# Performance work log

Hardware: AMD Instinct MI355X
Metric: run time of the kernel (lower is better)

## Reference

```python
import jax, jax.numpy as jnp
import numpy as np

N_QUBITS = 8
N_LAYERS = 2


def _apply_1q_shared(state, U, q):
    # state: [B, 2,2,...,2]; U: [2,2] complex, applied to qubit q (axis q+1)
    state = jnp.moveaxis(state, q + 1, -1)
    state = jnp.einsum('ij,...j->...i', U, state)
    return jnp.moveaxis(state, -1, q + 1)


def _apply_1q_batched(state, U, q):
    # U: [B,2,2], per-sample gate on qubit q
    state = jnp.moveaxis(state, q + 1, -1)
    state = jnp.einsum('bij,b...j->b...i', U, state)
    return jnp.moveaxis(state, -1, q + 1)


def _apply_cnot(state, c, t):
    ca, ta = c + 1, t + 1
    s0 = jnp.take(state, 0, axis=ca)
    s1 = jnp.take(state, 1, axis=ca)
    ta_shift = ta - 1 if ta > ca else ta  # axis index after removing control axis
    s1 = jnp.flip(s1, axis=ta_shift)
    return jnp.stack([s0, s1], axis=ca)


def _rot_matrix(phi, theta, omega):
    # PennyLane Rot = RZ(omega) @ RY(theta) @ RZ(phi)
    c = jnp.cos(theta / 2).astype(jnp.complex64)
    s = jnp.sin(theta / 2).astype(jnp.complex64)
    ep = jnp.exp(-0.5j * (phi + omega).astype(jnp.complex64))
    em = jnp.exp(-0.5j * (phi - omega).astype(jnp.complex64))
    return jnp.stack([
        jnp.stack([ep * c, -jnp.conj(em) * s]),
        jnp.stack([em * s, jnp.conj(ep) * c]),
    ])


def _quantum_layer(angles, qw):
    # angles: [B, n_qubits] float; qw: [n_layers, n_qubits, 3]
    B, n = angles.shape[0], N_QUBITS
    state = jnp.zeros((B, 2 ** n), jnp.complex64).at[:, 0].set(1.0)
    state = state.reshape((B,) + (2,) * n)
    # AngleEmbedding (rotation='X'): RX(angle_q) on wire q, per-sample angle
    c = jnp.cos(angles / 2).astype(jnp.complex64)  # [B, n]
    s = (-1j * jnp.sin(angles / 2)).astype(jnp.complex64)
    for q in range(n):
        U = jnp.stack([
            jnp.stack([c[:, q], s[:, q]], -1),
            jnp.stack([s[:, q], c[:, q]], -1),
        ], -2)  # [B,2,2]
        state = _apply_1q_batched(state, U, q)
    # StronglyEntanglingLayers
    for l in range(N_LAYERS):
        for q in range(n):
            U = _rot_matrix(qw[l, q, 0], qw[l, q, 1], qw[l, q, 2])
            state = _apply_1q_shared(state, U, q)
        r = (l % (n - 1)) + 1
        for q in range(n):
            state = _apply_cnot(state, q, (q + r) % n)
    # <Z_i> expectations: wire 0 is MSB of the flattened index
    probs = jnp.abs(state.reshape(B, 2 ** n)) ** 2  # [B, 2^n]
    idx = jnp.arange(2 ** n)
    bits = (idx[None, :] >> (n - 1 - jnp.arange(n)[:, None])) & 1  # [n, 2^n]
    signs = (1.0 - 2.0 * bits).astype(probs.dtype)
    return probs @ signs.T  # [B, n]


def setup_inputs() -> dict:
    key = jax.random.key(0)
    ks = jax.random.split(key, 8)
    B, D_IN, D_OUT, H = 65536, 17, 32, 64
    x = jax.random.normal(ks[0], (B, D_IN), jnp.float32)
    Wp = jax.random.normal(ks[1], (N_QUBITS, D_IN), jnp.float32) / np.sqrt(D_IN)
    bp = jnp.zeros((N_QUBITS,), jnp.float32)
    qw = jax.random.uniform(ks[2], (N_LAYERS, N_QUBITS, 3), jnp.float32) * (2 * np.pi)
    W1 = jax.random.normal(ks[3], (H, N_QUBITS), jnp.float32) / np.sqrt(N_QUBITS)
    b1 = jnp.zeros((H,), jnp.float32)
    W2 = jax.random.normal(ks[4], (D_OUT, H), jnp.float32) / np.sqrt(H)
    b2 = jnp.zeros((D_OUT,), jnp.float32)
    return {"x": x, "Wp": Wp, "bp": bp, "qw": qw, "W1": W1, "b1": b1, "W2": W2, "b2": b2}


def reference(x, Wp, bp, qw, W1, b1, W2, b2):
    angles = x @ Wp.T + bp            # input_projection: [B, n_qubits]
    z = _quantum_layer(angles, qw)    # [B, n_qubits]
    h = jax.nn.relu(z @ W1.T + b1)    # [B, 64]
    return jnp.tanh(h @ W2.T + b2)    # [B, 32]
```

## Files before the change

kernel.cpp:

```cpp
#include <hip/hip_runtime.h>
#include <hip/hip_bf16.h>
#include <math.h>


#define DEVINL __device__ __forceinline__

struct Pau { unsigned x, z; int ph; };
constexpr int pcnt8(unsigned v){ int c=0; for(int i=0;i<8;++i) c+=(v>>i)&1; return c; }
constexpr Pau pmul(Pau a, Pau b){
  return Pau{a.x^b.x, a.z^b.z, (a.ph + b.ph + 2*pcnt8(a.z & b.x)) & 3};
}
constexpr Pau conjP(int j, int a){
  Pau X{ j<7 ? ((1u<<j)|(1u<<(j+1))) : 0x83u, 0u, 0 };
  Pau Z{ 0u, j>0 ? ((2u<<j)-1u) : 0xFEu, 0 };
  if (a==0) return X;
  if (a==2) return Z;
  Pau y = pmul(X, Z);
  return Pau{y.x, y.z, (y.ph+1)&3};
}
constexpr unsigned SQM[8] = {0x54,0xA8,0x05,0x0A,0x15,0x2A,0x55,0xAA};
constexpr int TPREF[9]   = {0,27,54,63,72,99,126,207,288};

struct TTab { unsigned char mx[288], my[288], mz[288]; signed char sg[288]; };
constexpr TTab gen_tt(){
  TTab T{};
  int t=0;
  for (int q=0;q<8;++q){
    int sup[8]={}; int m=0;
    for (int j=0;j<8;++j) if ((SQM[q]>>j)&1) sup[m++]=j;
    int nt=1; for (int i=0;i<m;++i) nt*=3;
    for (int a=0;a<nt;++a){
      Pau P{0u,0u,0}; int rem=a;
      for (int i=0;i<m;++i){ P = pmul(P, conjP(sup[i], rem%3)); rem/=3; }
      unsigned y = P.x & P.z;
      int tau = (P.ph + 3*pcnt8(y)) & 3;
      T.mx[t]=(unsigned char)(P.x & ~P.z);
      T.my[t]=(unsigned char)y;
      T.mz[t]=(unsigned char)(P.z & ~P.x);
      T.sg[t]=(signed char)(tau==0 ? 1 : -1);
      ++t;
    }
  }
  return T;
}
constexpr TTab TT = gen_tt();

struct cpx { float r, i; };
DEVINL cpx cmul(cpx a, cpx b){ return {a.r*b.r - a.i*b.i, a.r*b.i + a.i*b.r}; }
DEVINL cpx cconj(cpx a){ return {a.r, -a.i}; }
DEVINL cpx cadd(cpx a, cpx b){ return {a.r+b.r, a.i+b.i}; }

DEVINL void buildR(const float* qw3, cpx R[2][2]){
  float phi=qw3[0], th=qw3[1], om=qw3[2], s,c,sp,cp,sm,cm;
  sincosf(0.5f*th,&s,&c);
  sincosf(0.5f*(phi+om),&sp,&cp);
  sincosf(0.5f*(phi-om),&sm,&cm);
  R[0][0]={cp*c,-sp*c}; R[0][1]={-cm*s,-sm*s};
  R[1][0]={cm*s,-sm*s}; R[1][1]={cp*c, sp*c};
}
DEVINL void conjH(const cpx R[2][2], const cpx S[2][2], cpx H[2][2]){
  cpx M[2][2];
  for (int i=0;i<2;++i) for (int j=0;j<2;++j)
    M[i][j] = cadd(cmul(S[i][0],R[0][j]), cmul(S[i][1],R[1][j]));
  for (int i=0;i<2;++i) for (int j=0;j<2;++j)
    H[i][j] = cadd(cmul(cconj(R[0][i]),M[0][j]), cmul(cconj(R[1][i]),M[1][j]));
}

__global__ void prep_kernel(const float* __restrict__ qw, float* __restrict__ ws){
  __shared__ float n_sh[8][3];
  const int tid = threadIdx.x;
  if (tid < 8){
    const int q = tid;
    cpx R1[2][2], R2[2][2], H[2][2];
    buildR(qw + q*3,      R1);
    buildR(qw + 24 + q*3, R2);
    const cpx SX[2][2] = {{{0,0},{1,0}},{{1,0},{0,0}}};
    const cpx SY[2][2] = {{{0,0},{0,-1}},{{0,1},{0,0}}};
    const cpx SZ[2][2] = {{{1,0},{0,0}},{{0,0},{-1,0}}};
    conjH(R1,SX,H); ws[q*6+0] = -H[0][1].i; ws[q*6+3] = H[0][0].r;
    conjH(R1,SY,H); ws[q*6+1] = -H[0][1].i; ws[q*6+4] = H[0][0].r;
    conjH(R1,SZ,H); ws[q*6+2] = -H[0][1].i; ws[q*6+5] = H[0][0].r;
    conjH(R2,SZ,H);
    n_sh[q][0] = H[0][1].r;
    n_sh[q][1] = -H[0][1].i;
    n_sh[q][2] = H[0][0].r;
  }
  __syncthreads();
  if (tid < 288){
    int q = 0;
    while (tid >= TPREF[q+1]) ++q;
    int rem = tid - TPREF[q];
    float coef = (float)TT.sg[tid];
    unsigned m = SQM[q];
    while (m){
      int j = __ffs(m) - 1; m &= m - 1;
      coef *= n_sh[j][rem % 3];
      rem /= 3;
    }
    ws[48 + tid] = coef;
  }
}

DEVINL float tanh_fast(float v){
  float e = __expf(2.f*v);
  return 1.f - 2.f/(e + 1.f);
}

__global__ __launch_bounds__(256)
void qnet_pauli(const float* __restrict__ x, const float* __restrict__ Wp,
                const float* __restrict__ bp, const float* __restrict__ ws,
                const float* __restrict__ W1, const float* __restrict__ b1,
                const float* __restrict__ W2, const float* __restrict__ b2,
                float* __restrict__ out, int B){
  __shared__ __align__(16) float smem[3136 + 256*17];
  float* sws = smem;
  float* sWp = smem + 336;
  float* sbp = smem + 472;
  float* sW1 = smem + 480;
  float* sb1 = smem + 992;
  float* sW2 = smem + 1056;
  float* sb2 = smem + 3104;
  float* shx = smem + 3136;

  const int tid = threadIdx.x;
  const int b   = blockIdx.x*256 + tid;

  for (int i = tid; i < 336;  i += 256) sws[i] = ws[i];
  for (int i = tid; i < 136;  i += 256) sWp[i] = Wp[i];
  if (tid < 8)  sbp[tid] = bp[tid];
  for (int i = tid; i < 512;  i += 256) sW1[i] = W1[i];
  if (tid < 64) sb1[tid] = b1[tid];
  for (int i = tid; i < 2048; i += 256) sW2[i] = W2[i];
  if (tid < 32) sb2[tid] = b2[tid];

  const int base = blockIdx.x*256*17;
  const int lim  = B*17 - base;
#pragma unroll
  for (int i = 0; i < 17; ++i){
    int o = i*256 + tid;
    if (o < lim) shx[o] = x[base + o];
  }
  __syncthreads();
  if (b >= B) return;

  float rx[8], ry[8], rz[8];
  {
    float xv[17];
#pragma unroll
    for (int k=0;k<17;++k) xv[k] = shx[tid*17 + k];
#pragma unroll
    for (int q=0;q<8;++q){
      float ang = sbp[q];
#pragma unroll
      for (int k=0;k<17;++k) ang = fmaf(xv[k], sWp[q*17+k], ang);
      float sa, ca;
      __sincosf(ang, &sa, &ca);
      rx[q] = ca*sws[q*6+3] - sa*sws[q*6+0];
      ry[q] = ca*sws[q*6+4] - sa*sws[q*6+1];
      rz[q] = ca*sws[q*6+5] - sa*sws[q*6+2];
    }
  }

  const float* cf = sws + 48;
  float zz[8];
#pragma unroll
  for (int q=0;q<8;++q){
    float acc = 0.f;
#pragma unroll
    for (int t=TPREF[q]; t<TPREF[q+1]; ++t){
      float p = cf[t];
#pragma unroll
      for (int j=0;j<8;++j){
        if (TT.mx[t] & (1u<<j)) p *= rx[j];
        if (TT.my[t] & (1u<<j)) p *= ry[j];
        if (TT.mz[t] & (1u<<j)) p *= rz[j];
      }
      acc += p;
    }
    zz[q] = acc;
  }

  float acc[32];
#pragma unroll
  for (int j=0;j<32;++j) acc[j] = sb2[j];

#pragma unroll
  for (int lc=0; lc<4; ++lc){
    float h16[16];
#pragma unroll
    for (int i=0;i<16;++i){
      const int l = lc*16 + i;
      const float4* w1p = (const float4*)(sW1 + l*8);
      float4 wA = w1p[0], wB = w1p[1];
      float hl = sb1[l];
      hl = fmaf(zz[0], wA.x, hl); hl = fmaf(zz[1], wA.y, hl);
      hl = fmaf(zz[2], wA.z, hl); hl = fmaf(zz[3], wA.w, hl);
      hl = fmaf(zz[4], wB.x, hl); hl = fmaf(zz[5], wB.y, hl);
      hl = fmaf(zz[6], wB.z, hl); hl = fmaf(zz[7], wB.w, hl);
      h16[i] = fmaxf(hl, 0.f);
    }
#pragma unroll
    for (int j=0;j<32;++j){
      const float4* w2p = (const float4*)(sW2 + j*64 + lc*16);
      float4 wa = w2p[0], wb = w2p[1], wc = w2p[2], wd = w2p[3];
      float a = acc[j];
      a = fmaf(h16[ 0], wa.x, a); a = fmaf(h16[ 1], wa.y, a);
      a = fmaf(h16[ 2], wa.z, a); a = fmaf(h16[ 3], wa.w, a);
      a = fmaf(h16[ 4], wb.x, a); a = fmaf(h16[ 5], wb.y, a);
      a = fmaf(h16[ 6], wb.z, a); a = fmaf(h16[ 7], wb.w, a);
      a = fmaf(h16[ 8], wc.x, a); a = fmaf(h16[ 9], wc.y, a);
      a = fmaf(h16[10], wc.z, a); a = fmaf(h16[11], wc.w, a);
      a = fmaf(h16[12], wd.x, a); a = fmaf(h16[13], wd.y, a);
      a = fmaf(h16[14], wd.z, a); a = fmaf(h16[15], wd.w, a);
      acc[j] = a;
    }
  }

  float4* op4 = (float4*)(out + (size_t)b*32);
#pragma unroll
  for (int jj=0;jj<8;++jj){
    float4 v;
    v.x = tanh_fast(acc[jj*4+0]);
    v.y = tanh_fast(acc[jj*4+1]);
    v.z = tanh_fast(acc[jj*4+2]);
    v.w = tanh_fast(acc[jj*4+3]);
    op4[jj] = v;
  }
}

extern "C" void kernel_launch(void* const* d_in, const int* in_sizes, int n_in,
                              void* d_out, int out_size, void* d_ws, size_t ws_size,
                              hipStream_t stream) {
  const float* x  = (const float*)d_in[0];
  const float* Wp = (const float*)d_in[1];
  const float* bp = (const float*)d_in[2];
  const float* qw = (const float*)d_in[3];
  const float* W1 = (const float*)d_in[4];
  const float* b1 = (const float*)d_in[5];
  const float* W2 = (const float*)d_in[6];
  const float* b2 = (const float*)d_in[7];
  float* out = (float*)d_out;
  const int B = in_sizes[0] / 17;

  prep_kernel<<<1, 288, 0, stream>>>(qw, (float*)d_ws);
  qnet_pauli<<<(B + 255)/256, 256, 0, stream>>>(x, Wp, bp, (const float*)d_ws,
                                                W1, b1, W2, b2, out, B);
}
```

Measured before the change: 101.0 us.

## Split each sample's work across four waves with shared-memory handoff

Each block now handles 64 samples with 256 threads. The four waves each take a quarter of the angle projections, Pauli-term products, hidden units and output columns, and pass partial results through LDS between phases. Output is staged in padded LDS so global stores are coalesced. The goal is to cut per-thread register pressure, which should raise occupancy and improve store coalescing. The cost is four extra block barriers, reloading the weight tables into LDS four times as often, and more shared-memory traffic.

```diff
diff --git a/kernel.cpp b/kernel.cpp
--- a/kernel.cpp
+++ b/kernel.cpp
@@ -45,6 +45,26 @@
 }
 constexpr TTab TT = gen_tt();
 
+constexpr int qof(int t){
+  return (t<27)?0:(t<54)?1:(t<63)?2:(t<72)?3:(t<99)?4:(t<126)?5:(t<207)?6:7;
+}
+
+template<int T0, int T1>
+DEVINL void terms_range(const float* __restrict__ cf, const float rx[8],
+                        const float ry[8], const float rz[8], float zp[8]){
+#pragma unroll
+  for (int t=T0; t<T1; ++t){
+    float p = cf[t];
+#pragma unroll
+    for (int j=0;j<8;++j){
+      if (TT.mx[t] & (1u<<j)) p *= rx[j];
+      if (TT.my[t] & (1u<<j)) p *= ry[j];
+      if (TT.mz[t] & (1u<<j)) p *= rz[j];
+    }
+    zp[qof(t)] += p;
+  }
+}
+
 struct cpx { float r, i; };
 DEVINL cpx cmul(cpx a, cpx b){ return {a.r*b.r - a.i*b.i, a.r*b.i + a.i*b.r}; }
 DEVINL cpx cconj(cpx a){ return {a.r, -a.i}; }
@@ -112,120 +132,129 @@
                 const float* __restrict__ W1, const float* __restrict__ b1,
                 const float* __restrict__ W2, const float* __restrict__ b2,
                 float* __restrict__ out, int B){
-  __shared__ __align__(16) float smem[3136 + 256*17];
-  float* sws = smem;
+  __shared__ __align__(16) float smem[9536];
+  float* sA  = smem;
   float* sWp = smem + 336;
   float* sbp = smem + 472;
   float* sW1 = smem + 480;
   float* sb1 = smem + 992;
   float* sW2 = smem + 1056;
   float* sb2 = smem + 3104;
-  float* shx = smem + 3136;
+  float* X   = smem + 3136;
+  float* pzz = X;
+  float* sbl = X + 2304;
+  float* sx  = X + 3840;
+  float* sh  = X + 2304;
+  float* sout= X;
 
   const int tid = threadIdx.x;
-  const int b   = blockIdx.x*256 + tid;
-
-  for (int i = tid; i < 336;  i += 256) sws[i] = ws[i];
+  const int l   = tid & 63;
+  const int w   = tid >> 6;
+
+  for (int i = tid; i < 336;  i += 256) sA[i]  = ws[i];
   for (int i = tid; i < 136;  i += 256) sWp[i] = Wp[i];
   if (tid < 8)  sbp[tid] = bp[tid];
   for (int i = tid; i < 512;  i += 256) sW1[i] = W1[i];
   if (tid < 64) sb1[tid] = b1[tid];
   for (int i = tid; i < 2048; i += 256) sW2[i] = W2[i];
   if (tid < 32) sb2[tid] = b2[tid];
-
-  const int base = blockIdx.x*256*17;
-  const int lim  = B*17 - base;
-#pragma unroll
-  for (int i = 0; i < 17; ++i){
-    int o = i*256 + tid;
-    if (o < lim) shx[o] = x[base + o];
-  }
-  __syncthreads();
-  if (b >= B) return;
-
-  float rx[8], ry[8], rz[8];
+  const int xbase = blockIdx.x * (64*17);
+  const int xlim  = B*17 - xbase;
+  for (int i = tid; i < 64*17; i += 256)
+    if (i < xlim) sx[i] = x[xbase + i];
+  __syncthreads();
+
   {
     float xv[17];
 #pragma unroll
-    for (int k=0;k<17;++k) xv[k] = shx[tid*17 + k];
-#pragma unroll
-    for (int q=0;q<8;++q){
+    for (int k=0;k<17;++k) xv[k] = sx[l*17+k];
+#pragma unroll
+    for (int e=0;e<2;++e){
+      const int q = 2*w + e;
       float ang = sbp[q];
-#pragma unroll
-      for (int k=0;k<17;++k) ang = fmaf(xv[k], sWp[q*17+k], ang);
+      const float* wp = sWp + q*17;
+#pragma unroll
+      for (int k=0;k<17;++k) ang = fmaf(xv[k], wp[k], ang);
       float sa, ca;
       __sincosf(ang, &sa, &ca);
-      rx[q] = ca*sws[q*6+3] - sa*sws[q*6+0];
-      ry[q] = ca*sws[q*6+4] - sa*sws[q*6+1];
-      rz[q] = ca*sws[q*6+5] - sa*sws[q*6+2];
-    }
-  }
-
-  const float* cf = sws + 48;
-  float zz[8];
-#pragma unroll
-  for (int q=0;q<8;++q){
-    float acc = 0.f;
-#pragma unroll
-    for (int t=TPREF[q]; t<TPREF[q+1]; ++t){
-      float p = cf[t];
-#pragma unroll
-      for (int j=0;j<8;++j){
-        if (TT.mx[t] & (1u<<j)) p *= rx[j];
-        if (TT.my[t] & (1u<<j)) p *= ry[j];
-        if (TT.mz[t] & (1u<<j)) p *= rz[j];
+      const float* Aq = sA + q*6;
+      sbl[       q*64 + l] = ca*Aq[3] - sa*Aq[0];
+      sbl[ 512 + q*64 + l] = ca*Aq[4] - sa*Aq[1];
+      sbl[1024 + q*64 + l] = ca*Aq[5] - sa*Aq[2];
+    }
+  }
+  __syncthreads();
+
+  {
+    float rx[8], ry[8], rz[8];
+#pragma unroll
+    for (int q=0;q<8;++q){
+      rx[q] = sbl[       q*64 + l];
+      ry[q] = sbl[ 512 + q*64 + l];
+      rz[q] = sbl[1024 + q*64 + l];
+    }
+    float zp[8] = {0,0,0,0,0,0,0,0};
+    const float* cf = sA + 48;
+    if      (w==0) terms_range<  0, 72>(cf, rx,ry,rz, zp);
+    else if (w==1) terms_range< 72,144>(cf, rx,ry,rz, zp);
+    else if (w==2) terms_range<144,216>(cf, rx,ry,rz, zp);
+    else           terms_range<216,288>(cf, rx,ry,rz, zp);
+    float* pz = pzz + w*576 + l*9;
+#pragma unroll
+    for (int q=0;q<8;++q) pz[q] = zp[q];
+  }
+  __syncthreads();
+
+  {
+    float zzv[8];
+#pragma unroll
+    for (int q=0;q<8;++q)
+      zzv[q] = pzz[l*9+q] + pzz[576 + l*9+q] + pzz[1152 + l*9+q] + pzz[1728 + l*9+q];
+#pragma unroll
+    for (int i=0;i<16;++i){
+      const int hq = 16*w + i;
+      const float4* w1p = (const float4*)(sW1 + hq*8);
+      float4 wA = w1p[0], wB = w1p[1];
+      float hl = sb1[hq];
+      hl = fmaf(zzv[0], wA.x, hl); hl = fmaf(zzv[1], wA.y, hl);
+      hl = fmaf(zzv[2], wA.z, hl); hl = fmaf(zzv[3], wA.w, hl);
+      hl = fmaf(zzv[4], wB.x, hl); hl = fmaf(zzv[5], wB.y, hl);
+      hl = fmaf(zzv[6], wB.z, hl); hl = fmaf(zzv[7], wB.w, hl);
+      sh[hq*64 + l] = fmaxf(hl, 0.f);
+    }
+  }
+  __syncthreads();
+
+  {
+    const int j0 = 8*w;
+    float acc[8];
+#pragma unroll
+    for (int jj=0;jj<8;++jj) acc[jj] = sb2[j0+jj];
+#pragma unroll
+    for (int kc=0;kc<16;++kc){
+      float hk0 = sh[(4*kc+0)*64 + l];
+      float hk1 = sh[(4*kc+1)*64 + l];
+      float hk2 = sh[(4*kc+2)*64 + l];
+      float hk3 = sh[(4*kc+3)*64 + l];
+#pragma unroll
+      for (int jj=0;jj<8;++jj){
+        const float4 wv = *(const float4*)(sW2 + (j0+jj)*64 + 4*kc);
+        float a = acc[jj];
+        a = fmaf(hk0, wv.x, a); a = fmaf(hk1, wv.y, a);
+        a = fmaf(hk2, wv.z, a); a = fmaf(hk3, wv.w, a);
+        acc[jj] = a;
       }
-      acc += p;
-    }
-    zz[q] = acc;
-  }
-
-  float acc[32];
-#pragma unroll
-  for (int j=0;j<32;++j) acc[j] = sb2[j];
-
-#pragma unroll
-  for (int lc=0; lc<4; ++lc){
-    float h16[16];
-#pragma unroll
-    for (int i=0;i<16;++i){
-      const int l = lc*16 + i;
-      const float4* w1p = (const float4*)(sW1 + l*8);
-      float4 wA = w1p[0], wB = w1p[1];
-      float hl = sb1[l];
-      hl = fmaf(zz[0], wA.x, hl); hl = fmaf(zz[1], wA.y, hl);
-      hl = fmaf(zz[2], wA.z, hl); hl = fmaf(zz[3], wA.w, hl);
-      hl = fmaf(zz[4], wB.x, hl); hl = fmaf(zz[5], wB.y, hl);
-      hl = fmaf(zz[6], wB.z, hl); hl = fmaf(zz[7], wB.w, hl);
-      h16[i] = fmaxf(hl, 0.f);
-    }
-#pragma unroll
-    for (int j=0;j<32;++j){
-      const float4* w2p = (const float4*)(sW2 + j*64 + lc*16);
-      float4 wa = w2p[0], wb = w2p[1], wc = w2p[2], wd = w2p[3];
-      float a = acc[j];
-      a = fmaf(h16[ 0], wa.x, a); a = fmaf(h16[ 1], wa.y, a);
-      a = fmaf(h16[ 2], wa.z, a); a = fmaf(h16[ 3], wa.w, a);
-      a = fmaf(h16[ 4], wb.x, a); a = fmaf(h16[ 5], wb.y, a);
-      a = fmaf(h16[ 6], wb.z, a); a = fmaf(h16[ 7], wb.w, a);
-      a = fmaf(h16[ 8], wc.x, a); a = fmaf(h16[ 9], wc.y, a);
-      a = fmaf(h16[10], wc.z, a); a = fmaf(h16[11], wc.w, a);
-      a = fmaf(h16[12], wd.x, a); a = fmaf(h16[13], wd.y, a);
-      a = fmaf(h16[14], wd.z, a); a = fmaf(h16[15], wd.w, a);
-      acc[j] = a;
-    }
-  }
-
-  float4* op4 = (float4*)(out + (size_t)b*32);
-#pragma unroll
-  for (int jj=0;jj<8;++jj){
-    float4 v;
-    v.x = tanh_fast(acc[jj*4+0]);
-    v.y = tanh_fast(acc[jj*4+1]);
-    v.z = tanh_fast(acc[jj*4+2]);
-    v.w = tanh_fast(acc[jj*4+3]);
-    op4[jj] = v;
-  }
+    }
+#pragma unroll
+    for (int jj=0;jj<8;++jj)
+      sout[l*33 + j0 + jj] = tanh_fast(acc[jj]);
+  }
+  __syncthreads();
+
+  const int obase = blockIdx.x * 2048;
+  const int olim  = B*32 - obase;
+  for (int i = tid; i < 2048; i += 256)
+    if (i < olim) out[obase + i] = sout[(i>>5)*33 + (i&31)];
 }
 
 extern "C" void kernel_launch(void* const* d_in, const int* in_sizes, int n_in,
@@ -243,6 +272,6 @@
   const int B = in_sizes[0] / 17;
 
   prep_kernel<<<1, 288, 0, stream>>>(qw, (float*)d_ws);
-  qnet_pauli<<<(B + 255)/256, 256, 0, stream>>>(x, Wp, bp, (const float*)d_ws,
-                                                W1, b1, W2, b2, out, B);
-}
+  qnet_pauli<<<(B + 63)/64, 256, 0, stream>>>(x, Wp, bp, (const float*)d_ws,
+                                              W1, b1, W2, b2, out, B);
+}
```

New measurement: 89.41 us. 11.5% less time.
